# Kernel tuning notes

Hardware: AMD Instinct MI355X
Metric: run time of the kernel (lower is better)

## Reference

```python
import jax, jax.numpy as jnp
import numpy as np

STATE_DIM = 2048
OBS_DIM = 512
STEPS = 8192
PROC_STD = 0.1 ** 0.5   # sqrt(process_noise_var)
OBS_STD = 0.5 ** 0.5    # sqrt(observation_noise_var)


def setup_inputs() -> dict:
    key = jax.random.key(0)
    k1, k2, k3, k4, k5 = jax.random.split(key, 5)
    initial_state = jax.random.normal(k1, (STATE_DIM,), dtype=jnp.float32)
    process_noise = jax.random.normal(k2, (STEPS, STATE_DIM), dtype=jnp.float32)
    obs_noise = jax.random.normal(k3, (STEPS, OBS_DIM), dtype=jnp.float32)
    # Near-stable transition matrix (torch default is exactly identity, which is
    # marginally stable; keep spectral radius < 1 for an 8192-step rollout).
    A = 0.99 * jnp.eye(STATE_DIM, dtype=jnp.float32) \
        + 1e-4 * jax.random.normal(k4, (STATE_DIM, STATE_DIM), dtype=jnp.float32)
    C = 0.02 * jax.random.normal(k5, (OBS_DIM, STATE_DIM), dtype=jnp.float32)
    return {
        "initial_state": initial_state,
        "A": A,
        "C": C,
        "process_noise": process_noise,
        "obs_noise": obs_noise,
        "steps": STEPS,
    }


def reference(initial_state, A, C, process_noise, obs_noise, steps):
    # obs_t   = C @ state_t + obs_noise_t   * sqrt(obs_var)
    # state_{t+1} = A @ state_t + proc_noise_t * sqrt(proc_var)
    def step(state, noises):
        pn, on = noises
        obs = C @ state + on * OBS_STD
        new_state = A @ state + pn * PROC_STD
        return new_state, obs

    _, observations = jax.lax.scan(step, initial_state, (process_noise, obs_noise))
    return observations  # (steps, obs_dim)
```

## Files before the change

kernel.cpp:

```cpp
#include <hip/hip_runtime.h>


#define SD 2048
#define OD 512
#define NT 8192
#define BLK 64
#define KB 128
#define KBP (KB+16)
#define NP 7
#define NPH 6
#define NPN 5
#define PROC_STD 0.31622776601683794f
#define OBS_STD  0.7071067811865476f

typedef __attribute__((ext_vector_type(8))) short v8s;
typedef __attribute__((ext_vector_type(4))) float v4f;

__device__ __forceinline__ unsigned short f2bf(float f) {
    union { float f; unsigned int u; } v; v.f = f;
    unsigned int r = v.u + 0x7fffu + ((v.u >> 16) & 1u);
    return (unsigned short)(r >> 16);
}
__device__ __forceinline__ float bf2f(unsigned short u) {
    union { unsigned int ui; float f; } cv; cv.ui = (unsigned int)u << 16;
    return cv.f;
}

#define GLD16(g, l) __builtin_amdgcn_global_load_lds( \
    (const __attribute__((address_space(1))) unsigned int*)(g), \
    (__attribute__((address_space(3))) unsigned int*)(l), 16, 0, 0)


__device__ __forceinline__ void body_g64(unsigned short* SH,
        const unsigned short* __restrict__ A,
        const unsigned short* __restrict__ B, int ldb,
        int tM, int tN, int mode,
        unsigned short* __restrict__ obf, int ldo,
        float* __restrict__ o32,
        const unsigned short* __restrict__ X1,
        const unsigned short* __restrict__ X2,
        const unsigned short* __restrict__ X3,
        unsigned short* __restrict__ Pout,
        float c1, float c2, float c3) {
    unsigned short* Al = SH;
    unsigned short* Xt = SH + 64 * 40;
    int tid = threadIdx.x, lane = tid & 63, w = tid >> 6;
    int m16 = lane & 15, q = lane >> 4;
    int ar = tid >> 2, ao = (tid & 3) * 8;
    int xk = tid >> 3, xn = (tid & 7) * 8;
    int qb = xk >> 3;
    v4f acc[4] = {{0,0,0,0},{0,0,0,0},{0,0,0,0},{0,0,0,0}};

    v8s av = *(const v8s*)(A + (size_t)(tM + ar) * SD + ao);
    v8s xv = *(const v8s*)(B + (size_t)xk * ldb + tN + xn);
    for (int k0 = 0; k0 < SD; k0 += 32) {
        *(v8s*)(Al + ar * 40 + ao) = av;
#pragma unroll
        for (int c = 0; c < 8; ++c) {
            int n = xn + c, sw = (n >> 3) & 3;
            Xt[n * 40 + (((qb ^ sw) << 3) | (xk & 7))] = xv[c];
        }
        __syncthreads();
        if (k0 + 32 < SD) {
            av = *(const v8s*)(A + (size_t)(tM + ar) * SD + (k0 + 32) + ao);
            xv = *(const v8s*)(B + (size_t)(k0 + 32 + xk) * ldb + tN + xn);
        }
        v8s a = *(const v8s*)(Al + (w * 16 + m16) * 40 + q * 8);
#pragma unroll
        for (int c = 0; c < 4; ++c) {
            int nl = c * 16 + m16, swn = (nl >> 3) & 3;
            v8s b = *(const v8s*)(Xt + nl * 40 + ((q ^ swn) << 3));
            acc[c] = __builtin_amdgcn_mfma_f32_16x16x32_bf16(a, b, acc[c], 0, 0, 0);
        }
        __syncthreads();
    }
#pragma unroll
    for (int c = 0; c < 4; ++c)
#pragma unroll
        for (int j = 0; j < 4; ++j) {
            int r = tM + w * 16 + q * 4 + j;
            int col = tN + c * 16 + m16;
            float v = acc[c][j];
            size_t iS = (size_t)r * SD + col;
            if (mode == 2) {
                v += c1 * bf2f(X1[iS]) + c2 * bf2f(X2[iS]) + c3 * bf2f(X3[iS]);
                obf[iS] = f2bf(v);
            } else if (mode == 3) {
                v = c1 * bf2f(X1[iS]) + v;
                obf[iS] = f2bf(v);
            } else if (mode == 4) {
                obf[iS] = f2bf(v);
                Pout[iS] = f2bf(c1 * bf2f(X1[iS]) + c2 * bf2f(X2[iS]) + c3 * v);
            } else if (mode == 1) {
                o32[(size_t)r * ldo + col] = v;
            } else {
                obf[(size_t)r * ldo + col] = f2bf(v);
            }
        }
}

__device__ __forceinline__ void body_horner(unsigned short* SH, int bx,
        const unsigned short* __restrict__ Abf,
        const unsigned short* __restrict__ Xbf,
        const float* __restrict__ Wp,
        float* __restrict__ X32o,
        unsigned short* __restrict__ Xbfo,
        int initShift) {
    unsigned short* Al = SH;
    unsigned short* Xt = SH + 32 * 72;
    int tM = (bx & 63) * 32, tN = (bx >> 6) * 32;
    int tid = threadIdx.x, lane = tid & 63, w = tid >> 6;
    int m16 = lane & 15, q = lane >> 4;
    int ar = tid >> 3, ao = (tid & 7) * 8;
    int xk = tid >> 2, xn = (tid & 3) * 8;
    int qb = xk >> 3;
    v4f acc = {0, 0, 0, 0};
    v8s av = *(const v8s*)(Abf + (size_t)(tM + ar) * SD + ao);
    v8s xv = *(const v8s*)(Xbf + (size_t)xk * KB + tN + xn);
    int nl = (w & 1) * 16 + m16;
    int swn = (nl >> 3) & 3;
    int rl = (w >> 1) * 16 + m16;
    for (int k0 = 0; k0 < SD; k0 += 64) {
        *(v8s*)(Al + ar * 72 + ao) = av;
#pragma unroll
        for (int c = 0; c < 8; ++c) {
            int n = xn + c, sw = (n >> 3) & 3;
            Xt[n * 72 + (((qb ^ sw) << 3) | (xk & 7))] = xv[c];
        }
        __syncthreads();
        if (k0 + 64 < SD) {
            av = *(const v8s*)(Abf + (size_t)(tM + ar) * SD + (k0 + 64) + ao);
            xv = *(const v8s*)(Xbf + (size_t)(k0 + 64 + xk) * KB + tN + xn);
        }
#pragma unroll
        for (int ch = 0; ch < 2; ++ch) {
            v8s a = *(const v8s*)(Al + rl * 72 + ch * 32 + q * 8);
            int q2 = ch * 4 + q;
            v8s b = *(const v8s*)(Xt + nl * 72 + ((q2 ^ swn) << 3));
            acc = __builtin_amdgcn_mfma_f32_16x16x32_bf16(a, b, acc, 0, 0, 0);
        }
        __syncthreads();
    }
#pragma unroll
    for (int j = 0; j < 4; ++j) {
        int r = tM + (w >> 1) * 16 + q * 4 + j;
        int kc = tN + (w & 1) * 16 + m16;
        float v = acc[j] + Wp[r * KB + kc];
        if (initShift) {
            if (kc < 127) {
                X32o[r * KB + kc + 1] = v;
                Xbfo[(size_t)r * KBP + kc + 17] = f2bf(v);
            }
        } else {
            X32o[r * KB + kc] = v;
            if (Xbfo) Xbfo[r * KB + kc] = f2bf(v);
        }
    }
}

__device__ __forceinline__ void body_scan(unsigned short* SH, int bx,
        const unsigned short* __restrict__ Mrbf,
        const unsigned short* __restrict__ Sbf_in,
        const float* __restrict__ S32_in,
        float* __restrict__ S32_out,
        unsigned short* __restrict__ Sbf_out,
        float ar, int shift) {
    unsigned short* Al = SH;
    unsigned short* Xt = SH + 32 * 72;
    int tM = (bx & 63) * 32, tN = (bx >> 6) * 32;
    int tid = threadIdx.x, lane = tid & 63, w = tid >> 6;
    int m16 = lane & 15, q = lane >> 4;
    int ar_ = tid >> 3, ao = (tid & 7) * 8;
    int xk = tid >> 2, xn = (tid & 3) * 8;
    int qb = xk >> 3;
    int coff = tN + xn + 16 - shift;
    v4f acc = {0, 0, 0, 0};
    v8s av = *(const v8s*)(Mrbf + (size_t)(tM + ar_) * SD + ao);
    v8s xv = *(const v8s*)(Sbf_in + (size_t)xk * KBP + coff);
    int nl = (w & 1) * 16 + m16;
    int swn = (nl >> 3) & 3;
    int rl = (w >> 1) * 16 + m16;
    for (int k0 = 0; k0 < SD; k0 += 64) {
        *(v8s*)(Al + ar_ * 72 + ao) = av;
#pragma unroll
        for (int c = 0; c < 8; ++c) {
            int n = xn + c, sw = (n >> 3) & 3;
            Xt[n * 72 + (((qb ^ sw) << 3) | (xk & 7))] = xv[c];
        }
        __syncthreads();
        if (k0 + 64 < SD) {
            av = *(const v8s*)(Mrbf + (size_t)(tM + ar_) * SD + (k0 + 64) + ao);
            xv = *(const v8s*)(Sbf_in + (size_t)(k0 + 64 + xk) * KBP + coff);
        }
#pragma unroll
        for (int ch = 0; ch < 2; ++ch) {
            v8s a = *(const v8s*)(Al + rl * 72 + ch * 32 + q * 8);
            int q2 = ch * 4 + q;
            v8s b = *(const v8s*)(Xt + nl * 72 + ((q2 ^ swn) << 3));
            acc = __builtin_amdgcn_mfma_f32_16x16x32_bf16(a, b, acc, 0, 0, 0);
        }
        __syncthreads();
    }
#pragma unroll
    for (int j = 0; j < 4; ++j) {
        int r = tM + (w >> 1) * 16 + q * 4 + j;
        int kc = tN + (w & 1) * 16 + m16;
        int idx = r * KB + kc;
        int ksh = kc - shift;
        float v = S32_in[idx] + acc[j] + (ksh >= 0 ? ar * S32_in[r * KB + ksh] : 0.f);
        S32_out[idx] = v;
        Sbf_out[(size_t)r * KBP + kc + 16] = f2bf(v);
    }
}

__device__ __forceinline__ void body_g128(unsigned short* SH, int bid,
        const unsigned short* __restrict__ Aptr, int lda,
        const unsigned short* __restrict__ Bptr, int ldb,
        int mtiles, int npx,
        unsigned short* __restrict__ obf, size_t ldo) {
    unsigned short* As = SH;
    unsigned short* Bs = SH + 4096;
    int tid = threadIdx.x, lane = tid & 63, w = tid >> 6;
    int mT = (bid >> 3) % mtiles;
    int nT = (bid & 7) * npx + (bid >> 3) / mtiles;
    int tM = mT * 128, tN = nT * 128;
    int wr = w >> 1, wc = w & 1;
    int m16 = lane & 15, q = lane >> 4;
    int srow = lane >> 2, sk8 = lane & 3;
    const unsigned short* ga0 = Aptr + (size_t)(tM + w * 16 + srow) * lda + sk8 * 8;
    const unsigned short* ga1 = ga0 + (size_t)64 * lda;
    const unsigned short* gb0 = Bptr + (size_t)(tN + w * 16 + srow) * ldb + sk8 * 8;
    const unsigned short* gb1 = gb0 + (size_t)64 * ldb;
    unsigned short* la0 = As + w * 512;
    unsigned short* la1 = As + 2048 + w * 512;
    unsigned short* lb0 = Bs + w * 512;
    unsigned short* lb1 = Bs + 2048 + w * 512;

    v4f acc[4][4];
#pragma unroll
    for (int mi = 0; mi < 4; ++mi)
#pragma unroll
        for (int ni = 0; ni < 4; ++ni) acc[mi][ni] = (v4f){0, 0, 0, 0};

    GLD16(ga0, la0); GLD16(ga1, la1); GLD16(gb0, lb0); GLD16(gb1, lb1);
    ga0 += 32; ga1 += 32; gb0 += 32; gb1 += 32;
    __syncthreads();

    int arow = (wr * 64 + m16) * 32 + q * 8;
    int brow = (wc * 64 + m16) * 32 + q * 8;
    for (int k0 = 0; k0 < SD; k0 += 32) {
        v8s a[4], b[4];
#pragma unroll
        for (int mi = 0; mi < 4; ++mi) a[mi] = *(const v8s*)(As + arow + mi * 512);
#pragma unroll
        for (int ni = 0; ni < 4; ++ni) b[ni] = *(const v8s*)(Bs + brow + ni * 512);
        __syncthreads();
        if (k0 + 32 < SD) {
            GLD16(ga0, la0); GLD16(ga1, la1); GLD16(gb0, lb0); GLD16(gb1, lb1);
            ga0 += 32; ga1 += 32; gb0 += 32; gb1 += 32;
        }
#pragma unroll
        for (int mi = 0; mi < 4; ++mi)
#pragma unroll
            for (int ni = 0; ni < 4; ++ni)
                acc[mi][ni] = __builtin_amdgcn_mfma_f32_16x16x32_bf16(a[mi], b[ni],
                                                                      acc[mi][ni], 0, 0, 0);
        __syncthreads();
    }
#pragma unroll
    for (int mi = 0; mi < 4; ++mi)
#pragma unroll
        for (int ni = 0; ni < 4; ++ni)
#pragma unroll
            for (int j = 0; j < 4; ++j) {
                int row = tM + wr * 64 + mi * 16 + q * 4 + j;
                int col = tN + wc * 64 + ni * 16 + m16;
                obf[(size_t)row * ldo + col] = f2bf(acc[mi][ni][j]);
            }
}


__device__ double d_binom(int m, int p) {
    if (p < 0 || p > m) return 0.0;
    double c = 1.0;
    for (int q = 1; q <= p; ++q) c = c * (double)(m - p + q) / (double)q;
    return c;
}
__device__ double d_p99(int n) {
    double r = 1.0;
    for (int q = 0; q < n; ++q) r *= 0.99;
    return r;
}

__global__ __launch_bounds__(256) void k_prepAll(const float* __restrict__ A,
                                                 const float* __restrict__ C,
                                                 unsigned short* __restrict__ Ebf,
                                                 unsigned short* __restrict__ Cbf,
                                                 float* __restrict__ wW,
                                                 float* __restrict__ cW,
                                                 unsigned short* __restrict__ Tbf) {
    int bid = blockIdx.x;
    if (bid < 16384) {
        int idx = bid * 256 + threadIdx.x;
        int r = idx >> 11, c = idx & 2047;
        float e = A[idx] - (r == c ? 0.99f : 0.0f);
        Ebf[idx] = f2bf(e);
    } else if (bid < 20480) {
        int idx = (bid - 16384) * 256 + threadIdx.x;
        Cbf[idx] = f2bf(C[idx]);
    } else {
        int idx = (bid - 20480) * 256 + threadIdx.x;
        if (idx < NP * 64) {
            int p = idx >> 6, j = idx & 63;
            int m = 63 - j;
            wW[idx] = (p <= m) ? (float)((double)PROC_STD * d_binom(m, p) * d_p99(m - p)) : 0.f;
            cW[idx] = (p <= j) ? (float)(d_binom(j, p) * d_p99(j - p)) : 0.f;
        }
        if (idx < NP * 64 * 64) {
            int p = idx >> 12, j = (idx >> 6) & 63, i = idx & 63;
            int mm = i - 1 - j;
            float t = (mm >= p) ? (float)((double)PROC_STD * d_binom(mm, p) * d_p99(mm - p)) : 0.f;
            Tbf[idx] = f2bf(t);
        }
    }
}

__global__ __launch_bounds__(256) void k_wsum(const float* __restrict__ pn,
                                              const float* __restrict__ wW,
                                              float* __restrict__ W32,
                                              unsigned short* __restrict__ Wbf,
                                              unsigned short* __restrict__ Vbf,
                                              unsigned short* __restrict__ pnbf) {
    __shared__ float ws[NP * 64];
    int tid = threadIdx.x;
    for (int t = tid; t < NP * 64; t += 256) ws[t] = wW[t];
    __syncthreads();
    int bx = blockIdx.x;
    int k = bx >> 1, dc = bx & 1;
    int d0 = dc * 1024 + tid * 4;
    float acc[NP][4];
#pragma unroll
    for (int p = 0; p < NP; ++p)
#pragma unroll
        for (int u = 0; u < 4; ++u) acc[p][u] = 0.f;
    for (int j = 0; j < 64; ++j) {
        size_t gi = (size_t)(k * BLK + j) * SD + d0;
        float4 v = *(const float4*)(pn + gi);
        ushort4 b4;
        b4.x = f2bf(v.x); b4.y = f2bf(v.y); b4.z = f2bf(v.z); b4.w = f2bf(v.w);
        *(ushort4*)(pnbf + gi) = b4;
#pragma unroll
        for (int p = 0; p < NP; ++p) {
            float wv = ws[p * 64 + j];
            acc[p][0] += wv * v.x; acc[p][1] += wv * v.y;
            acc[p][2] += wv * v.z; acc[p][3] += wv * v.w;
        }
    }
#pragma unroll
    for (int jj = 0; jj < 3; ++jj)
#pragma unroll
        for (int u = 0; u < 4; ++u) {
            W32[((size_t)jj * SD + d0 + u) * KB + k] = acc[2 * jj][u];
            Wbf[((size_t)jj * SD + d0 + u) * KB + k] = f2bf(acc[2 * jj + 1][u]);
        }
#pragma unroll
    for (int u = 0; u < 4; ++u)
        Vbf[(size_t)(d0 + u) * KB + k] = f2bf(acc[6][u]);
}

__global__ __launch_bounds__(256) void k_nn_ce(const unsigned short* __restrict__ L,
                                               const unsigned short* __restrict__ X,
                                               unsigned short* __restrict__ NNout,
                                               const unsigned short* __restrict__ CEa,
                                               const unsigned short* __restrict__ CEb,
                                               unsigned short* __restrict__ CEout,
                                               int mode,
                                               unsigned short* __restrict__ Pout,
                                               const unsigned short* __restrict__ X1,
                                               const unsigned short* __restrict__ X2,
                                               float c1, float c2, float c3) {
    __shared__ __align__(16) unsigned short SH[5120];
    int bid = blockIdx.x;
    if (bid < 1024)
        body_g64(SH, L, X, SD, (bid & 31) * 64, (bid >> 5) * 64, mode, NNout, SD,
                 nullptr, X1, X2, nullptr, Pout, c1, c2, c3);
    else {
        int bx = bid - 1024;
        body_g64(SH, CEa, CEb, SD, (bx & 7) * 64, (bx >> 3) * 64, 0, CEout, SD,
                 nullptr, nullptr, nullptr, nullptr, nullptr, 0.f, 0.f, 0.f);
    }
}

__global__ __launch_bounds__(256) void k_M_Y(const unsigned short* __restrict__ E3,
                                             const unsigned short* __restrict__ P,
                                             const unsigned short* __restrict__ Ebf,
                                             const unsigned short* __restrict__ E2,
                                             unsigned short* __restrict__ Mbf,
                                             float c1, float c2, float c3,
                                             const unsigned short* __restrict__ Wbf,
                                             const float* __restrict__ W32,
                                             float* __restrict__ Y32) {
    __shared__ __align__(16) unsigned short SH[5120];
    int bid = blockIdx.x;
    if (bid < 1024)
        body_g64(SH, E3, P, SD, (bid & 31) * 64, (bid >> 5) * 64, 2, Mbf, SD,
                 nullptr, Ebf, E2, E3, nullptr, c1, c2, c3);
    else {
        int l = bid - 1024;
        int j = l >> 8, bx = l & 255;
        body_horner(SH, bx, Ebf, Wbf + (size_t)j * SD * KB, W32 + (size_t)j * SD * KB,
                    Y32 + (size_t)j * SD * KB, nullptr, 0);
    }
}

__global__ __launch_bounds__(256) void k_ce2_z(const unsigned short* __restrict__ CEall,
                                               const unsigned short* __restrict__ E2,
                                               const float* __restrict__ Y32,
                                               const unsigned short* __restrict__ Vbf0,
                                               float* __restrict__ V32o,
                                               unsigned short* __restrict__ Vbfo) {
    __shared__ __align__(16) unsigned short SH[5120];
    int bid = blockIdx.x;
    if (bid < 512) {
        int y = bid >> 8, bx = bid & 255;
        body_g64(SH, CEall + (size_t)(1 + y) * OD * SD, E2, SD,
                 (bx & 7) * 64, (bx >> 3) * 64, 0,
                 (unsigned short*)(CEall + (size_t)(3 + y) * OD * SD), SD,
                 nullptr, nullptr, nullptr, nullptr, nullptr, 0.f, 0.f, 0.f);
    } else
        body_horner(SH, bid - 512, E2, Vbf0, Y32 + (size_t)2 * SD * KB, V32o, Vbfo, 0);
}

__global__ __launch_bounds__(256) void k_ce1_z(const unsigned short* __restrict__ CEall,
                                               const unsigned short* __restrict__ E2,
                                               const float* __restrict__ Y32,
                                               const unsigned short* __restrict__ Vbf1,
                                               float* __restrict__ V32o,
                                               unsigned short* __restrict__ Vbfo) {
    __shared__ __align__(16) unsigned short SH[5120];
    int bid = blockIdx.x;
    if (bid < 256)
        body_g64(SH, CEall + (size_t)3 * OD * SD, E2, SD,
                 (bid & 7) * 64, (bid >> 3) * 64, 0,
                 (unsigned short*)(CEall + (size_t)5 * OD * SD), SD,
                 nullptr, nullptr, nullptr, nullptr, nullptr, 0.f, 0.f, 0.f);
    else
        body_horner(SH, bid - 256, E2, Vbf1, Y32 + (size_t)SD * KB, V32o, Vbfo, 0);
}

__global__ __launch_bounds__(256) void k_hornerZI(const unsigned short* __restrict__ E2,
                                                  const unsigned short* __restrict__ Vbf0,
                                                  const float* __restrict__ Y32,
                                                  const float* __restrict__ s0,
                                                  float* __restrict__ S32,
                                                  unsigned short* __restrict__ Sbf0,
                                                  unsigned short* __restrict__ Sbf1) {
    __shared__ __align__(16) unsigned short SH[5120];
    int bid = blockIdx.x;
    if (bid < 256)
        body_horner(SH, bid, E2, Vbf0, Y32, S32, Sbf0, 1);
    else {
        int idx = (bid - 256) * 256 + threadIdx.x;
        int d = idx >> 4, c = idx & 15;
        Sbf0[(size_t)d * KBP + c] = 0;
        Sbf1[(size_t)d * KBP + c] = 0;
        if (c == 0) {
            float v = s0[d];
            S32[d * KB] = v;
            Sbf0[(size_t)d * KBP + 16] = f2bf(v);
        }
    }
}

__global__ __launch_bounds__(256) void k_sqscan(const unsigned short* __restrict__ Lbf,
                                                unsigned short* __restrict__ Mbfo,
                                                float twoa,
                                                const unsigned short* __restrict__ Sbf_in,
                                                const float* __restrict__ S32_in,
                                                float* __restrict__ S32_out,
                                                unsigned short* __restrict__ Sbf_out,
                                                float ar, int shift) {
    __shared__ __align__(16) unsigned short SH[5120];
    int bid = blockIdx.x;
    if (bid < 1024)
        body_g64(SH, Lbf, Lbf, SD, (bid & 31) * 64, (bid >> 5) * 64, 3, Mbfo, SD,
                 nullptr, Lbf, nullptr, nullptr, nullptr, twoa, 0.f, 0.f);
    else
        body_scan(SH, bid - 1024, Lbf, Sbf_in, S32_in, S32_out, Sbf_out, ar, shift);
}

__global__ __launch_bounds__(256) void k_pall_s(const unsigned short* __restrict__ CEall,
                                                const unsigned short* __restrict__ pnbf,
                                                unsigned short* __restrict__ Pall,
                                                const unsigned short* __restrict__ M4,
                                                const unsigned short* __restrict__ Sbf_in,
                                                const float* __restrict__ S32_in,
                                                float* __restrict__ S32_out,
                                                unsigned short* __restrict__ Sbf_out,
                                                float ar) {
    __shared__ __align__(16) unsigned short SH[8192];
    int bid = blockIdx.x;
    if (bid < 1280)
        body_g128(SH, bid, CEall, SD, pnbf, SD, 20, 8, Pall, (size_t)NT);
    else
        body_scan(SH, bid - 1280, M4, Sbf_in, S32_in, S32_out, Sbf_out, ar, 8);
}

__global__ __launch_bounds__(256) void k_G(const unsigned short* __restrict__ CEall,
                                           const unsigned short* __restrict__ Sbf16,
                                           float* __restrict__ G) {
    __shared__ __align__(16) unsigned short SH[5120];
    int l = blockIdx.x;
    int y = l >> 4, bx = l & 15;
    body_g64(SH, CEall + (size_t)y * OD * SD, Sbf16, KBP,
             (bx & 7) * 64, (bx >> 3) * 64, 1, nullptr, KB,
             G + (size_t)y * OD * KB, nullptr, nullptr, nullptr, nullptr, 0.f, 0.f, 0.f);
}

__global__ __launch_bounds__(256) void k_final2(const unsigned short* __restrict__ P,
                                                const unsigned short* __restrict__ Tbf,
                                                const float* __restrict__ G,
                                                const float* __restrict__ cW,
                                                const float* __restrict__ on,
                                                float* __restrict__ out, float af) {
    __shared__ __align__(16) float obsT[64][65];
    unsigned short* Al = (unsigned short*)obsT;
    unsigned short* Xt = Al + 64 * 40;
    int bx = blockIdx.x;
    int kb = bx >> 3, ob = bx & 7;
    int o0 = ob * 64;
    int tid = threadIdx.x, lane = tid & 63, w = tid >> 6;
    int m16 = lane & 15, q = lane >> 4;
    int ar = tid >> 2, ao = (tid & 3) * 8;
    int xk = tid >> 3, xn = (tid & 7) * 8;
    int qb = xk >> 3;
    v4f acc[4] = {{0,0,0,0},{0,0,0,0},{0,0,0,0},{0,0,0,0}};
    const unsigned short* Abase = P + (size_t)kb * 64;

    v8s av = *(const v8s*)(Abase + (size_t)(o0 + ar) * NT + ao);
    v8s xv = *(const v8s*)(Tbf + xk * 64 + xn);
    for (int kc = 0; kc < 2 * NPN; ++kc) {
        *(v8s*)(Al + ar * 40 + ao) = av;
#pragma unroll
        for (int c = 0; c < 8; ++c) {
            int n = xn + c, sw = (n >> 3) & 3;
            Xt[n * 40 + (((qb ^ sw) << 3) | (xk & 7))] = xv[c];
        }
        __syncthreads();
        if (kc + 1 < 2 * NPN) {
            int p = (kc + 1) >> 1, j0 = ((kc + 1) & 1) * 32;
            av = *(const v8s*)(Abase + (size_t)(p * OD + o0 + ar) * NT + j0 + ao);
            xv = *(const v8s*)(Tbf + p * 4096 + (j0 + xk) * 64 + xn);
        }
        v8s a = *(const v8s*)(Al + (w * 16 + m16) * 40 + q * 8);
#pragma unroll
        for (int c = 0; c < 4; ++c) {
            int nl = c * 16 + m16, swn = (nl >> 3) & 3;
            v8s b = *(const v8s*)(Xt + nl * 40 + ((q ^ swn) << 3));
            acc[c] = __builtin_amdgcn_mfma_f32_16x16x32_bf16(a, b, acc[c], 0, 0, 0);
        }
        __syncthreads();
    }
#pragma unroll
    for (int c = 0; c < 4; ++c)
#pragma unroll
        for (int j = 0; j < 4; ++j)
            obsT[w * 16 + q * 4 + j][c * 16 + m16] = acc[c][j];
    __syncthreads();
    int g = tid >> 6;
    float Hv[NPH];
#pragma unroll
    for (int p = 0; p < NPH; ++p) {
        size_t base = ((size_t)p * OD + o0 + lane) * KB + kb;
        Hv[p] = G[base] + (kb >= 16 ? af * G[base - 16] : 0.f);
    }
#pragma unroll
    for (int r = 0; r < 16; ++r) {
        int trow = r * 4 + g;
        float a2 = obsT[lane][trow];
#pragma unroll
        for (int p = 0; p < NPH; ++p) a2 += cW[p * 64 + trow] * Hv[p];
        size_t oidx = (size_t)(kb * 64 + trow) * OD + o0 + lane;
        out[oidx] = a2 + OBS_STD * on[oidx];
    }
}

extern "C" void kernel_launch(void* const* d_in, const int* in_sizes, int n_in,
                              void* d_out, int out_size, void* d_ws, size_t ws_size,
                              hipStream_t stream) {
    const float* s0 = (const float*)d_in[0];
    const float* A  = (const float*)d_in[1];
    const float* C  = (const float*)d_in[2];
    const float* pn = (const float*)d_in[3];
    const float* on = (const float*)d_in[4];
    float* out = (float*)d_out;

    char* p = (char*)d_ws;
    auto take = [&](size_t n) { char* r = p; p += (n + 255) & ~(size_t)255; return r; };
    unsigned short* Ebf = (unsigned short*)take((size_t)SD * SD * 2);
    unsigned short* CEall = (unsigned short*)take((size_t)NPH * OD * SD * 2);
    unsigned short* Pall = (unsigned short*)take((size_t)(NPN * OD) * NT * 2);
    unsigned short* Xp0 = (unsigned short*)take((size_t)SD * SD * 2);
    unsigned short* Xp1 = (unsigned short*)take((size_t)SD * SD * 2);
    unsigned short* Xp2 = (unsigned short*)take((size_t)SD * SD * 2);
    unsigned short* Mbf = (unsigned short*)take((size_t)SD * SD * 2);
    float* W32          = (float*)take((size_t)3 * SD * KB * 4);
    unsigned short* Wbf = (unsigned short*)take((size_t)3 * SD * KB * 2);
    float* Y32          = (float*)take((size_t)3 * SD * KB * 4);
    float* V32[2] = {(float*)take((size_t)SD * KB * 4), (float*)take((size_t)SD * KB * 4)};
    unsigned short* Vbf[2] = {(unsigned short*)take((size_t)SD * KB * 2),
                              (unsigned short*)take((size_t)SD * KB * 2)};
    float* SC32[2] = {(float*)take((size_t)SD * KB * 4), (float*)take((size_t)SD * KB * 4)};
    unsigned short* SCbf[2] = {(unsigned short*)take((size_t)SD * KBP * 2),
                               (unsigned short*)take((size_t)SD * KBP * 2)};
    float* wW   = (float*)take((size_t)NP * 64 * 4);
    float* cW   = (float*)take((size_t)NP * 64 * 4);
    unsigned short* Tbf = (unsigned short*)take((size_t)NP * 64 * 64 * 2);
    unsigned short* pnbf = (unsigned short*)take((size_t)SD * NT * 2);
    float* G    = (float*)take((size_t)NPH * OD * KB * 4);

    double pw[65]; pw[0] = 1.0;
    for (int m = 1; m <= 64; ++m) pw[m] = pw[m - 1] * 0.99;
    const double bin[7] = {1, 64, 2016, 41664, 635376, 7624512, 74974368};
    float cf[7];
    for (int m = 1; m <= 6; ++m) cf[m] = (float)(bin[m] * pw[64 - m]);
    float a64 = (float)pw[64];

    k_prepAll<<<20592, 256, 0, stream>>>(A, C, Ebf, CEall, wW, cW, Tbf);
    k_wsum<<<256, 256, 0, stream>>>(pn, wW, W32, Wbf, Vbf[0], pnbf);
    k_nn_ce<<<1280, 256, 0, stream>>>(Ebf, Ebf, Xp0, CEall, Ebf, CEall + (size_t)OD * SD,
                                      0, nullptr, nullptr, nullptr, 0.f, 0.f, 0.f);
    k_nn_ce<<<1280, 256, 0, stream>>>(Ebf, Xp0, Xp1, CEall, Xp0,
                                      CEall + (size_t)2 * OD * SD,
                                      4, Xp2, Ebf, Xp0, cf[4], cf[5], cf[6]);
    k_M_Y<<<1792, 256, 0, stream>>>(Xp1, Xp2, Ebf, Xp0, Mbf, cf[1], cf[2], cf[3],
                                    Wbf, W32, Y32);
    k_ce2_z<<<768, 256, 0, stream>>>(CEall, Xp0, Y32, Vbf[0], V32[1], Vbf[1]);
    k_ce1_z<<<512, 256, 0, stream>>>(CEall, Xp0, Y32, Vbf[1], V32[0], Vbf[0]);
    k_hornerZI<<<384, 256, 0, stream>>>(Xp0, Vbf[0], Y32, s0, SC32[0], SCbf[0], SCbf[1]);
    float a = a64;
    k_sqscan<<<1280, 256, 0, stream>>>(Mbf, Xp0, 2.f * a,
                                       SCbf[0], SC32[0], SC32[1], SCbf[1], a, 1);
    a *= a;
    k_sqscan<<<1280, 256, 0, stream>>>(Xp0, Xp1, 2.f * a,
                                       SCbf[1], SC32[1], SC32[0], SCbf[0], a, 2);
    a *= a;
    k_sqscan<<<1280, 256, 0, stream>>>(Xp1, Xp0, 2.f * a,
                                       SCbf[0], SC32[0], SC32[1], SCbf[1], a, 4);
    a *= a;
    k_pall_s<<<1536, 256, 0, stream>>>(CEall, pnbf, Pall, Xp0,
                                       SCbf[1], SC32[1], SC32[0], SCbf[0], a);
    a *= a;
    k_G<<<96, 256, 0, stream>>>(CEall, SCbf[0] + 16, G);
    k_final2<<<1024, 256, 0, stream>>>(Pall, Tbf, G, cW, on, out, a);
}
```

Measured before the change: 760.1 us.

## Distribute Pall GEMM tiles as riders across earlier kernels and precompute weights on host

The large Pall GEMM (CE times bf16 process noise) is split into 128x128 tiles that ride along as extra blocks in the ce2, ce1, hornerZI and sqscan launches, so they fill idle CUs beside the latency-bound Horner/scan work. The final scan becomes a standalone kernel. NPN drops from 5 to 4 so Pall holds fewer rows. The wsum step is fused into the prep kernel, and the binomial weight tables are built on the host and copied with an async memcpy instead of a device kernel. The riders raise LDS use in those kernels and may compete with critical-path blocks.

```diff
diff --git a/kernel.cpp b/kernel.cpp
--- a/kernel.cpp
+++ b/kernel.cpp
@@ -1,4 +1,5 @@
 #include <hip/hip_runtime.h>
+#include <string.h>
 
 
 #define SD 2048
@@ -9,14 +10,14 @@
 #define KBP (KB+16)
 #define NP 7
 #define NPH 6
-#define NPN 5
+#define NPN 4
 #define PROC_STD 0.31622776601683794f
 #define OBS_STD  0.7071067811865476f
 
 typedef __attribute__((ext_vector_type(8))) short v8s;
 typedef __attribute__((ext_vector_type(4))) float v4f;
 
-__device__ __forceinline__ unsigned short f2bf(float f) {
+__device__ __host__ __forceinline__ unsigned short f2bf(float f) {
     union { float f; unsigned int u; } v; v.f = f;
     unsigned int r = v.u + 0x7fffu + ((v.u >> 16) & 1u);
     return (unsigned short)(r >> 16);
@@ -213,17 +214,13 @@
     }
 }
 
-__device__ __forceinline__ void body_g128(unsigned short* SH, int bid,
+__device__ __forceinline__ void body_g128(unsigned short* SH, int tM, int tN,
         const unsigned short* __restrict__ Aptr, int lda,
         const unsigned short* __restrict__ Bptr, int ldb,
-        int mtiles, int npx,
         unsigned short* __restrict__ obf, size_t ldo) {
     unsigned short* As = SH;
     unsigned short* Bs = SH + 4096;
     int tid = threadIdx.x, lane = tid & 63, w = tid >> 6;
-    int mT = (bid >> 3) % mtiles;
-    int nT = (bid & 7) * npx + (bid >> 3) / mtiles;
-    int tM = mT * 128, tN = nT * 128;
     int wr = w >> 1, wc = w & 1;
     int m16 = lane & 15, q = lane >> 4;
     int srow = lane >> 2, sk8 = lane & 3;
@@ -279,26 +276,67 @@
             }
 }
 
-
-__device__ double d_binom(int m, int p) {
-    if (p < 0 || p > m) return 0.0;
-    double c = 1.0;
-    for (int q = 1; q <= p; ++q) c = c * (double)(m - p + q) / (double)q;
-    return c;
-}
-__device__ double d_p99(int n) {
-    double r = 1.0;
-    for (int q = 0; q < n; ++q) r *= 0.99;
-    return r;
-}
-
-__global__ __launch_bounds__(256) void k_prepAll(const float* __restrict__ A,
-                                                 const float* __restrict__ C,
-                                                 unsigned short* __restrict__ Ebf,
-                                                 unsigned short* __restrict__ Cbf,
-                                                 float* __restrict__ wW,
-                                                 float* __restrict__ cW,
-                                                 unsigned short* __restrict__ Tbf) {
+__device__ __forceinline__ void pall_rider(unsigned short* SH, int pbid,
+        const unsigned short* __restrict__ CEall,
+        const unsigned short* __restrict__ pnbf,
+        unsigned short* __restrict__ Pall) {
+    int mT = pbid >> 6;
+    int local = pbid & 63;
+    int nT = (local & 7) * 8 + (local >> 3);
+    body_g128(SH, mT * 128, nT * 128, CEall, SD, pnbf, SD, Pall, (size_t)NT);
+}
+
+__device__ __forceinline__ void body_wsum(int bx, const float* __restrict__ pn,
+        const float* __restrict__ wW,
+        float* __restrict__ W32, unsigned short* __restrict__ Wbf,
+        unsigned short* __restrict__ Vbf, unsigned short* __restrict__ pnbf) {
+    __shared__ float ws[NP * 64];
+    int tid = threadIdx.x;
+    for (int t = tid; t < NP * 64; t += 256) ws[t] = wW[t];
+    __syncthreads();
+    int k = bx >> 1, dc = bx & 1;
+    int d0 = dc * 1024 + tid * 4;
+    float acc[NP][4];
+#pragma unroll
+    for (int p = 0; p < NP; ++p)
+#pragma unroll
+        for (int u = 0; u < 4; ++u) acc[p][u] = 0.f;
+    for (int j = 0; j < 64; ++j) {
+        size_t gi = (size_t)(k * BLK + j) * SD + d0;
+        float4 v = *(const float4*)(pn + gi);
+        ushort4 b4;
+        b4.x = f2bf(v.x); b4.y = f2bf(v.y); b4.z = f2bf(v.z); b4.w = f2bf(v.w);
+        *(ushort4*)(pnbf + gi) = b4;
+#pragma unroll
+        for (int p = 0; p < NP; ++p) {
+            float wv = ws[p * 64 + j];
+            acc[p][0] += wv * v.x; acc[p][1] += wv * v.y;
+            acc[p][2] += wv * v.z; acc[p][3] += wv * v.w;
+        }
+    }
+#pragma unroll
+    for (int jj = 0; jj < 3; ++jj)
+#pragma unroll
+        for (int u = 0; u < 4; ++u) {
+            W32[((size_t)jj * SD + d0 + u) * KB + k] = acc[2 * jj][u];
+            Wbf[((size_t)jj * SD + d0 + u) * KB + k] = f2bf(acc[2 * jj + 1][u]);
+        }
+#pragma unroll
+    for (int u = 0; u < 4; ++u)
+        Vbf[(size_t)(d0 + u) * KB + k] = f2bf(acc[6][u]);
+}
+
+
+__global__ __launch_bounds__(256) void k_prep(const float* __restrict__ A,
+                                              const float* __restrict__ C,
+                                              unsigned short* __restrict__ Ebf,
+                                              unsigned short* __restrict__ Cbf,
+                                              const float* __restrict__ pn,
+                                              const float* __restrict__ wW,
+                                              float* __restrict__ W32,
+                                              unsigned short* __restrict__ Wbf,
+                                              unsigned short* __restrict__ Vbf,
+                                              unsigned short* __restrict__ pnbf) {
     int bid = blockIdx.x;
     if (bid < 16384) {
         int idx = bid * 256 + threadIdx.x;
@@ -309,63 +347,8 @@
         int idx = (bid - 16384) * 256 + threadIdx.x;
         Cbf[idx] = f2bf(C[idx]);
     } else {
-        int idx = (bid - 20480) * 256 + threadIdx.x;
-        if (idx < NP * 64) {
-            int p = idx >> 6, j = idx & 63;
-            int m = 63 - j;
-            wW[idx] = (p <= m) ? (float)((double)PROC_STD * d_binom(m, p) * d_p99(m - p)) : 0.f;
-            cW[idx] = (p <= j) ? (float)(d_binom(j, p) * d_p99(j - p)) : 0.f;
-        }
-        if (idx < NP * 64 * 64) {
-            int p = idx >> 12, j = (idx >> 6) & 63, i = idx & 63;
-            int mm = i - 1 - j;
-            float t = (mm >= p) ? (float)((double)PROC_STD * d_binom(mm, p) * d_p99(mm - p)) : 0.f;
-            Tbf[idx] = f2bf(t);
-        }
-    }
-}
-
-__global__ __launch_bounds__(256) void k_wsum(const float* __restrict__ pn,
-                                              const float* __restrict__ wW,
-                                              float* __restrict__ W32,
-                                              unsigned short* __restrict__ Wbf,
-                                              unsigned short* __restrict__ Vbf,
-                                              unsigned short* __restrict__ pnbf) {
-    __shared__ float ws[NP * 64];
-    int tid = threadIdx.x;
-    for (int t = tid; t < NP * 64; t += 256) ws[t] = wW[t];
-    __syncthreads();
-    int bx = blockIdx.x;
-    int k = bx >> 1, dc = bx & 1;
-    int d0 = dc * 1024 + tid * 4;
-    float acc[NP][4];
-#pragma unroll
-    for (int p = 0; p < NP; ++p)
-#pragma unroll
-        for (int u = 0; u < 4; ++u) acc[p][u] = 0.f;
-    for (int j = 0; j < 64; ++j) {
-        size_t gi = (size_t)(k * BLK + j) * SD + d0;
-        float4 v = *(const float4*)(pn + gi);
-        ushort4 b4;
-        b4.x = f2bf(v.x); b4.y = f2bf(v.y); b4.z = f2bf(v.z); b4.w = f2bf(v.w);
-        *(ushort4*)(pnbf + gi) = b4;
-#pragma unroll
-        for (int p = 0; p < NP; ++p) {
-            float wv = ws[p * 64 + j];
-            acc[p][0] += wv * v.x; acc[p][1] += wv * v.y;
-            acc[p][2] += wv * v.z; acc[p][3] += wv * v.w;
-        }
-    }
-#pragma unroll
-    for (int jj = 0; jj < 3; ++jj)
-#pragma unroll
-        for (int u = 0; u < 4; ++u) {
-            W32[((size_t)jj * SD + d0 + u) * KB + k] = acc[2 * jj][u];
-            Wbf[((size_t)jj * SD + d0 + u) * KB + k] = f2bf(acc[2 * jj + 1][u]);
-        }
-#pragma unroll
-    for (int u = 0; u < 4; ++u)
-        Vbf[(size_t)(d0 + u) * KB + k] = f2bf(acc[6][u]);
+        body_wsum(bid - 20480, pn, wW, W32, Wbf, Vbf, pnbf);
+    }
 }
 
 __global__ __launch_bounds__(256) void k_nn_ce(const unsigned short* __restrict__ L,
@@ -418,8 +401,10 @@
                                                const float* __restrict__ Y32,
                                                const unsigned short* __restrict__ Vbf0,
                                                float* __restrict__ V32o,
-                                               unsigned short* __restrict__ Vbfo) {
-    __shared__ __align__(16) unsigned short SH[5120];
+                                               unsigned short* __restrict__ Vbfo,
+                                               const unsigned short* __restrict__ pnbf,
+                                               unsigned short* __restrict__ Pall) {
+    __shared__ __align__(16) unsigned short SH[8192];
     int bid = blockIdx.x;
     if (bid < 512) {
         int y = bid >> 8, bx = bid & 255;
@@ -427,8 +412,10 @@
                  (bx & 7) * 64, (bx >> 3) * 64, 0,
                  (unsigned short*)(CEall + (size_t)(3 + y) * OD * SD), SD,
                  nullptr, nullptr, nullptr, nullptr, nullptr, 0.f, 0.f, 0.f);
-    } else
+    } else if (bid < 768)
         body_horner(SH, bid - 512, E2, Vbf0, Y32 + (size_t)2 * SD * KB, V32o, Vbfo, 0);
+    else
+        pall_rider(SH, bid - 768, CEall, pnbf, Pall);
 }
 
 __global__ __launch_bounds__(256) void k_ce1_z(const unsigned short* __restrict__ CEall,
@@ -436,16 +423,20 @@
                                                const float* __restrict__ Y32,
                                                const unsigned short* __restrict__ Vbf1,
                                                float* __restrict__ V32o,
-                                               unsigned short* __restrict__ Vbfo) {
-    __shared__ __align__(16) unsigned short SH[5120];
+                                               unsigned short* __restrict__ Vbfo,
+                                               const unsigned short* __restrict__ pnbf,
+                                               unsigned short* __restrict__ Pall) {
+    __shared__ __align__(16) unsigned short SH[8192];
     int bid = blockIdx.x;
     if (bid < 256)
         body_g64(SH, CEall + (size_t)3 * OD * SD, E2, SD,
                  (bid & 7) * 64, (bid >> 3) * 64, 0,
                  (unsigned short*)(CEall + (size_t)5 * OD * SD), SD,
                  nullptr, nullptr, nullptr, nullptr, nullptr, 0.f, 0.f, 0.f);
+    else if (bid < 512)
+        body_horner(SH, bid - 256, E2, Vbf1, Y32 + (size_t)SD * KB, V32o, Vbfo, 0);
     else
-        body_horner(SH, bid - 256, E2, Vbf1, Y32 + (size_t)SD * KB, V32o, Vbfo, 0);
+        pall_rider(SH, 170 + bid - 512, CEall, pnbf, Pall);
 }
 
 __global__ __launch_bounds__(256) void k_hornerZI(const unsigned short* __restrict__ E2,
@@ -454,12 +445,15 @@
                                                   const float* __restrict__ s0,
                                                   float* __restrict__ S32,
                                                   unsigned short* __restrict__ Sbf0,
-                                                  unsigned short* __restrict__ Sbf1) {
-    __shared__ __align__(16) unsigned short SH[5120];
+                                                  unsigned short* __restrict__ Sbf1,
+                                                  const unsigned short* __restrict__ CEall,
+                                                  const unsigned short* __restrict__ pnbf,
+                                                  unsigned short* __restrict__ Pall) {
+    __shared__ __align__(16) unsigned short SH[8192];
     int bid = blockIdx.x;
     if (bid < 256)
         body_horner(SH, bid, E2, Vbf0, Y32, S32, Sbf0, 1);
-    else {
+    else if (bid < 384) {
         int idx = (bid - 256) * 256 + threadIdx.x;
         int d = idx >> 4, c = idx & 15;
         Sbf0[(size_t)d * KBP + c] = 0;
@@ -469,7 +463,8 @@
             S32[d * KB] = v;
             Sbf0[(size_t)d * KBP + 16] = f2bf(v);
         }
-    }
+    } else
+        pall_rider(SH, 340 + bid - 384, CEall, pnbf, Pall);
 }
 
 __global__ __launch_bounds__(256) void k_sqscan(const unsigned short* __restrict__ Lbf,
@@ -479,31 +474,30 @@
                                                 const float* __restrict__ S32_in,
                                                 float* __restrict__ S32_out,
                                                 unsigned short* __restrict__ Sbf_out,
-                                                float ar, int shift) {
-    __shared__ __align__(16) unsigned short SH[5120];
+                                                float ar, int shift,
+                                                const unsigned short* __restrict__ CEall,
+                                                const unsigned short* __restrict__ pnbf,
+                                                unsigned short* __restrict__ Pall,
+                                                int riderBase) {
+    __shared__ __align__(16) unsigned short SH[8192];
     int bid = blockIdx.x;
     if (bid < 1024)
         body_g64(SH, Lbf, Lbf, SD, (bid & 31) * 64, (bid >> 5) * 64, 3, Mbfo, SD,
                  nullptr, Lbf, nullptr, nullptr, nullptr, twoa, 0.f, 0.f);
+    else if (bid < 1280)
+        body_scan(SH, bid - 1024, Lbf, Sbf_in, S32_in, S32_out, Sbf_out, ar, shift);
     else
-        body_scan(SH, bid - 1024, Lbf, Sbf_in, S32_in, S32_out, Sbf_out, ar, shift);
-}
-
-__global__ __launch_bounds__(256) void k_pall_s(const unsigned short* __restrict__ CEall,
-                                                const unsigned short* __restrict__ pnbf,
-                                                unsigned short* __restrict__ Pall,
-                                                const unsigned short* __restrict__ M4,
-                                                const unsigned short* __restrict__ Sbf_in,
-                                                const float* __restrict__ S32_in,
-                                                float* __restrict__ S32_out,
-                                                unsigned short* __restrict__ Sbf_out,
-                                                float ar) {
-    __shared__ __align__(16) unsigned short SH[8192];
-    int bid = blockIdx.x;
-    if (bid < 1280)
-        body_g128(SH, bid, CEall, SD, pnbf, SD, 20, 8, Pall, (size_t)NT);
-    else
-        body_scan(SH, bid - 1280, M4, Sbf_in, S32_in, S32_out, Sbf_out, ar, 8);
+        pall_rider(SH, riderBase + bid - 1280, CEall, pnbf, Pall);
+}
+
+__global__ __launch_bounds__(256) void k_scanOnly(const unsigned short* __restrict__ Mrbf,
+                                                  const unsigned short* __restrict__ Sbf_in,
+                                                  const float* __restrict__ S32_in,
+                                                  float* __restrict__ S32_out,
+                                                  unsigned short* __restrict__ Sbf_out,
+                                                  float ar) {
+    __shared__ __align__(16) unsigned short SH[5120];
+    body_scan(SH, blockIdx.x, Mrbf, Sbf_in, S32_in, S32_out, Sbf_out, ar, 8);
 }
 
 __global__ __launch_bounds__(256) void k_G(const unsigned short* __restrict__ CEall,
@@ -585,6 +579,20 @@
     }
 }
 
+struct WBuf { float wW[NP * 64]; float cW[NP * 64]; unsigned short T[NP * 4096]; };
+
+static double h_binom(int m, int p) {
+    if (p < 0 || p > m) return 0.0;
+    double c = 1.0;
+    for (int q = 1; q <= p; ++q) c = c * (double)(m - p + q) / (double)q;
+    return c;
+}
+static double h_p99(int n) {
+    double r = 1.0;
+    for (int q = 0; q < n; ++q) r *= 0.99;
+    return r;
+}
+
 extern "C" void kernel_launch(void* const* d_in, const int* in_sizes, int n_in,
                               void* d_out, int out_size, void* d_ws, size_t ws_size,
                               hipStream_t stream) {
@@ -613,11 +621,29 @@
     float* SC32[2] = {(float*)take((size_t)SD * KB * 4), (float*)take((size_t)SD * KB * 4)};
     unsigned short* SCbf[2] = {(unsigned short*)take((size_t)SD * KBP * 2),
                                (unsigned short*)take((size_t)SD * KBP * 2)};
-    float* wW   = (float*)take((size_t)NP * 64 * 4);
-    float* cW   = (float*)take((size_t)NP * 64 * 4);
-    unsigned short* Tbf = (unsigned short*)take((size_t)NP * 64 * 64 * 2);
+    char* dWCT = take(sizeof(WBuf));
+    float* wW = (float*)dWCT;
+    float* cW = wW + NP * 64;
+    unsigned short* Tbf = (unsigned short*)(cW + NP * 64);
     unsigned short* pnbf = (unsigned short*)take((size_t)SD * NT * 2);
     float* G    = (float*)take((size_t)NPH * OD * KB * 4);
+
+    static WBuf hb;
+    for (int pp = 0; pp < NP; ++pp)
+        for (int j = 0; j < 64; ++j) {
+            int m = 63 - j;
+            hb.wW[pp * 64 + j] = (pp <= m)
+                ? (float)((double)PROC_STD * h_binom(m, pp) * h_p99(m - pp)) : 0.f;
+            hb.cW[pp * 64 + j] = (pp <= j)
+                ? (float)(h_binom(j, pp) * h_p99(j - pp)) : 0.f;
+            for (int i = 0; i < 64; ++i) {
+                int mm = i - 1 - j;
+                float t = (mm >= pp)
+                    ? (float)((double)PROC_STD * h_binom(mm, pp) * h_p99(mm - pp)) : 0.f;
+                hb.T[pp * 4096 + j * 64 + i] = f2bf(t);
+            }
+        }
+    hipMemcpyAsync(dWCT, &hb, sizeof(WBuf), hipMemcpyHostToDevice, stream);
 
     double pw[65]; pw[0] = 1.0;
     for (int m = 1; m <= 64; ++m) pw[m] = pw[m - 1] * 0.99;
@@ -626,8 +652,7 @@
     for (int m = 1; m <= 6; ++m) cf[m] = (float)(bin[m] * pw[64 - m]);
     float a64 = (float)pw[64];
 
-    k_prepAll<<<20592, 256, 0, stream>>>(A, C, Ebf, CEall, wW, cW, Tbf);
-    k_wsum<<<256, 256, 0, stream>>>(pn, wW, W32, Wbf, Vbf[0], pnbf);
+    k_prep<<<20736, 256, 0, stream>>>(A, C, Ebf, CEall, pn, wW, W32, Wbf, Vbf[0], pnbf);
     k_nn_ce<<<1280, 256, 0, stream>>>(Ebf, Ebf, Xp0, CEall, Ebf, CEall + (size_t)OD * SD,
                                       0, nullptr, nullptr, nullptr, 0.f, 0.f, 0.f);
     k_nn_ce<<<1280, 256, 0, stream>>>(Ebf, Xp0, Xp1, CEall, Xp0,
@@ -635,21 +660,24 @@
                                       4, Xp2, Ebf, Xp0, cf[4], cf[5], cf[6]);
     k_M_Y<<<1792, 256, 0, stream>>>(Xp1, Xp2, Ebf, Xp0, Mbf, cf[1], cf[2], cf[3],
                                     Wbf, W32, Y32);
-    k_ce2_z<<<768, 256, 0, stream>>>(CEall, Xp0, Y32, Vbf[0], V32[1], Vbf[1]);
-    k_ce1_z<<<512, 256, 0, stream>>>(CEall, Xp0, Y32, Vbf[1], V32[0], Vbf[0]);
-    k_hornerZI<<<384, 256, 0, stream>>>(Xp0, Vbf[0], Y32, s0, SC32[0], SCbf[0], SCbf[1]);
+    k_ce2_z<<<938, 256, 0, stream>>>(CEall, Xp0, Y32, Vbf[0], V32[1], Vbf[1], pnbf, Pall);
+    k_ce1_z<<<682, 256, 0, stream>>>(CEall, Xp0, Y32, Vbf[1], V32[0], Vbf[0], pnbf, Pall);
+    k_hornerZI<<<556, 256, 0, stream>>>(Xp0, Vbf[0], Y32, s0, SC32[0], SCbf[0], SCbf[1],
+                                        CEall, pnbf, Pall);
     float a = a64;
-    k_sqscan<<<1280, 256, 0, stream>>>(Mbf, Xp0, 2.f * a,
-                                       SCbf[0], SC32[0], SC32[1], SCbf[1], a, 1);
+    k_sqscan<<<1451, 256, 0, stream>>>(Mbf, Xp0, 2.f * a,
+                                       SCbf[0], SC32[0], SC32[1], SCbf[1], a, 1,
+                                       CEall, pnbf, Pall, 512);
     a *= a;
-    k_sqscan<<<1280, 256, 0, stream>>>(Xp0, Xp1, 2.f * a,
-                                       SCbf[1], SC32[1], SC32[0], SCbf[0], a, 2);
+    k_sqscan<<<1451, 256, 0, stream>>>(Xp0, Xp1, 2.f * a,
+                                       SCbf[1], SC32[1], SC32[0], SCbf[0], a, 2,
+                                       CEall, pnbf, Pall, 683);
     a *= a;
-    k_sqscan<<<1280, 256, 0, stream>>>(Xp1, Xp0, 2.f * a,
-                                       SCbf[0], SC32[0], SC32[1], SCbf[1], a, 4);
+    k_sqscan<<<1450, 256, 0, stream>>>(Xp1, Xp0, 2.f * a,
+                                       SCbf[0], SC32[0], SC32[1], SCbf[1], a, 4,
+                                       CEall, pnbf, Pall, 854);
     a *= a;
-    k_pall_s<<<1536, 256, 0, stream>>>(CEall, pnbf, Pall, Xp0,
-                                       SCbf[1], SC32[1], SC32[0], SCbf[0], a);
+    k_scanOnly<<<256, 256, 0, stream>>>(Xp0, SCbf[1], SC32[1], SC32[0], SCbf[0], a);
     a *= a;
     k_G<<<96, 256, 0, stream>>>(CEall, SCbf[0] + 16, G);
     k_final2<<<1024, 256, 0, stream>>>(Pall, Tbf, G, cW, on, out, a);
```

Result: slower. 1.004 ms (+32.1%).
